# Performance work log

Measured on AMD Instinct MI355X. Metric: run time of the kernel, lower is better.

Reference implementation:

```python
import jax, jax.numpy as jnp
import numpy as np

TEMP = 1.0  # composition softmax temperature

def _bank_topk(x, U, V, logits, top_k):
    # softmax over primitive logits, select top-k, renormalize, fused low-rank projection
    w = jax.nn.softmax(logits / TEMP)                     # [P]
    tw, ti = jax.lax.top_k(w, top_k)                      # [k], [k]
    tw = tw / tw.sum()
    Us = U[ti]                                            # [k, d_in, r]
    Vs = V[ti]                                            # [k, r, d_out]
    h = jnp.einsum('bsd,kdr->bksr', x, Us)                # low-rank bottleneck
    return jnp.einsum('bksr,kro,k->bso', h, Vs, tw)       # weighted fuse

def reference(x, q_U, q_V, k_U, k_V, v_U, v_V, q_logits, k_logits, v_logits, out_w, top_k):
    B, S, _ = x.shape
    H, D = 16, 64
    q = _bank_topk(x, q_U, q_V, q_logits, top_k)
    k = _bank_topk(x, k_U, k_V, k_logits, top_k)
    v = _bank_topk(x, v_U, v_V, v_logits, top_k)
    q = q.reshape(B, S, H, D).transpose(0, 2, 1, 3)       # [B,H,S,D]
    k = k.reshape(B, S, H, D).transpose(0, 2, 1, 3)
    v = v.reshape(B, S, H, D).transpose(0, 2, 1, 3)
    scale = 1.0 / jnp.sqrt(jnp.asarray(D, dtype=x.dtype))
    scores = jnp.einsum('bhqd,bhkd->bhqk', q, k) * scale  # [B,H,S,S]
    causal = jnp.triu(jnp.ones((S, S), dtype=bool), 1)
    scores = jnp.where(causal[None, None], jnp.finfo(x.dtype).min, scores)
    probs = jax.nn.softmax(scores, axis=-1)
    out = jnp.einsum('bhqk,bhkd->bhqd', probs, v)
    out = out.transpose(0, 2, 1, 3).reshape(B, S, H * D)
    return out @ out_w.T                                   # nn.Linear(H*D, d_model, bias=False)

def setup_inputs() -> dict:
    key = jax.random.key(0)
    ks = jax.random.split(key, 11)
    P, d, r = 16, 1024, 64
    B, S = 4, 1024
    f = jnp.float32
    inp = {
        'x': jax.random.normal(ks[0], (B, S, d), f),
        'q_U': jax.random.normal(ks[1], (P, d, r), f) * (1.0 / np.sqrt(d)),
        'q_V': jax.random.normal(ks[2], (P, r, d), f) * (1.0 / np.sqrt(r)),
        'k_U': jax.random.normal(ks[3], (P, d, r), f) * (1.0 / np.sqrt(d)),
        'k_V': jax.random.normal(ks[4], (P, r, d), f) * (1.0 / np.sqrt(r)),
        'v_U': jax.random.normal(ks[5], (P, d, r), f) * (1.0 / np.sqrt(d)),
        'v_V': jax.random.normal(ks[6], (P, r, d), f) * (1.0 / np.sqrt(r)),
        'q_logits': jax.random.normal(ks[7], (P,), f) * 0.01,
        'k_logits': jax.random.normal(ks[8], (P,), f) * 0.01,
        'v_logits': jax.random.normal(ks[9], (P,), f) * 0.01,
        'out_w': jax.random.normal(ks[10], (d, d), f) * (1.0 / np.sqrt(d)),
        'top_k': 4,
    }
    return inp
```

## Files before the change

### kernel.cpp

```cpp
#include <hip/hip_runtime.h>
#include <math.h>

#define D_MODEL 1024
#define RANK    64
#define PMAX    16
#define S_LEN   1024
#define HD      64
#define MROWS   4096
#define NHEAD   16
#define BATCH   4
#define KCMAX   (PMAX * RANK)

typedef short short8v __attribute__((ext_vector_type(8)));
typedef short short4v __attribute__((ext_vector_type(4)));
typedef float floatx4 __attribute__((ext_vector_type(4)));

typedef __attribute__((address_space(1))) const unsigned int* gptr_t;
typedef __attribute__((address_space(3))) unsigned int* lptr_t;
typedef __attribute__((address_space(3))) short* lds3s;

static __device__ __forceinline__ void async16(const void* g, void* l) {
    __builtin_amdgcn_global_load_lds((gptr_t)g, (lptr_t)l, 16, 0, 0);
}

static __device__ __forceinline__ short f2bf(float f) {
    unsigned int u = __float_as_uint(f);
    u = (u + 0x7fffu + ((u >> 16) & 1u)) >> 16;
    return (short)u;
}

__global__ void topk_weights_kernel(const float* __restrict__ ql,
                                    const float* __restrict__ kl,
                                    const float* __restrict__ vl,
                                    const int* __restrict__ topk,
                                    int* __restrict__ idx_out,
                                    float* __restrict__ w_out) {
    int bank = threadIdx.x;
    if (bank >= 3) return;
    const float* lg = (bank == 0) ? ql : (bank == 1) ? kl : vl;
    int K = *topk; if (K < 1) K = 1; if (K > PMAX) K = PMAX;
    float l[PMAX];
    for (int i = 0; i < PMAX; ++i) l[i] = lg[i];
    bool used[PMAX];
    for (int i = 0; i < PMAX; ++i) used[i] = false;
    int   sel_i[PMAX];
    float sel_l[PMAX];
    for (int j = 0; j < K; ++j) {
        int best = -1; float bv = -INFINITY;
        for (int i = 0; i < PMAX; ++i)
            if (!used[i] && l[i] > bv) { bv = l[i]; best = i; }
        used[best] = true; sel_i[j] = best; sel_l[j] = bv;
    }
    float mx = sel_l[0];
    float e[PMAX];
    float sum = 0.f;
    for (int j = 0; j < K; ++j) { e[j] = __expf(sel_l[j] - mx); sum += e[j]; }
    float inv = 1.f / sum;
    for (int j = 0; j < PMAX; ++j) {
        idx_out[bank * PMAX + j] = (j < K) ? sel_i[j] : 0;
        w_out[bank * PMAX + j]   = (j < K) ? e[j] * inv : 0.f;
    }
}

__global__ __launch_bounds__(256) void convert_bf16_kernel(
    const float* __restrict__ src, short* __restrict__ dst, int n4) {
    int i = blockIdx.x * 256 + threadIdx.x;
    if (i < n4) {
        float4 f = ((const float4*)src)[i];
        short4 o;
        o.x = f2bf(f.x); o.y = f2bf(f.y); o.z = f2bf(f.z); o.w = f2bf(f.w);
        ((short4*)dst)[i] = o;
    }
}

__global__ __launch_bounds__(256) void prep_uv_kernel(
    const float* __restrict__ qU, const float* __restrict__ kU,
    const float* __restrict__ vU,
    const float* __restrict__ qV, const float* __restrict__ kV,
    const float* __restrict__ vV,
    const int* __restrict__ idx, const float* __restrict__ wsel,
    const int* __restrict__ topk,
    short* __restrict__ Uc, short* __restrict__ Vt) {
    int z    = blockIdx.z;
    int j    = blockIdx.y;
    int tile = blockIdx.x;
    int t    = threadIdx.x;
    int K = *topk; if (K < 1) K = 1; if (K > PMAX) K = PMAX;
    if (j >= K) return;
    __shared__ float T[64][65];
    int bank = (z < 3) ? z : z - 3;
    int p = idx[bank * PMAX + j];

    if (z < 3) {
        const float* U = (bank == 0) ? qU : (bank == 1) ? kU : vU;
        const float* src = U + (size_t)p * D_MODEL * RANK;
        short* dst = Uc + (size_t)bank * D_MODEL * KCMAX;
        int r4 = (t & 15) * 4;
        int dl = t >> 4;
#pragma unroll
        for (int i = 0; i < 4; ++i) {
            int d = tile * 64 + i * 16 + dl;
            float4 f = *(const float4*)&src[(size_t)d * RANK + r4];
            short4 o;
            o.x = f2bf(f.x); o.y = f2bf(f.y); o.z = f2bf(f.z); o.w = f2bf(f.w);
            *(short4*)&dst[(size_t)d * KCMAX + j * 64 + r4] = o;
        }
    } else {
        const float* V = (bank == 0) ? qV : (bank == 1) ? kV : vV;
        float wj = wsel[bank * PMAX + j];
        const float* src = V + (size_t)p * RANK * D_MODEL;
        int n0 = tile * 64;
        int nl = t & 63, rq = t >> 6;
#pragma unroll
        for (int i = 0; i < 16; ++i) {
            int rl = i * 4 + rq;
            T[nl][rl] = src[(size_t)rl * D_MODEL + n0 + nl] * wj;
        }
        __syncthreads();
        short* dst = Vt + (size_t)bank * D_MODEL * KCMAX;
        int rr = t >> 2;
#pragma unroll
        for (int i = 0; i < 4; ++i) {
            int c = (t & 3) * 16 + i * 4;
            short4 o;
            o.x = f2bf(T[rr][c + 0]); o.y = f2bf(T[rr][c + 1]);
            o.z = f2bf(T[rr][c + 2]); o.w = f2bf(T[rr][c + 3]);
            *(short4*)&dst[(size_t)(n0 + rr) * KCMAX + j * 64 + c] = o;
        }
    }
}

static __device__ __forceinline__ void mfma_gemm_tile(
    const short* __restrict__ A, const short* __restrict__ B, int kl,
    int lda, int ldb, int m0, int n0, short* As, short* Bs, floatx4 acc[4][4]) {
    const int t    = threadIdx.x;
    const int w    = t >> 6;
    const int lane = t & 63;
    const int wm   = w & 1, wn = w >> 1;
    const int colL = lane & 15, quad = lane >> 4;
    const int srow  = lane >> 2;
    const int skoff = (lane & 3) * 8;

#pragma unroll
    for (int i = 0; i < 4; ++i)
#pragma unroll
        for (int j = 0; j < 4; ++j) acc[i][j] = (floatx4){0.f, 0.f, 0.f, 0.f};

    for (int k0 = 0; k0 < kl; k0 += 32) {
        async16(A + (size_t)(m0 + w * 16 + srow) * lda + k0 + skoff,
                As + (w * 16 + srow) * 32 + skoff);
        async16(A + (size_t)(m0 + 64 + w * 16 + srow) * lda + k0 + skoff,
                As + (64 + w * 16 + srow) * 32 + skoff);
        async16(B + (size_t)(n0 + w * 16 + srow) * ldb + k0 + skoff,
                Bs + (w * 16 + srow) * 32 + skoff);
        async16(B + (size_t)(n0 + 64 + w * 16 + srow) * ldb + k0 + skoff,
                Bs + (64 + w * 16 + srow) * 32 + skoff);
        __syncthreads();
        short8v af[4], bf[4];
#pragma unroll
        for (int i = 0; i < 4; ++i)
            af[i] = *(const short8v*)&As[(wm * 64 + i * 16 + colL) * 32 + quad * 8];
#pragma unroll
        for (int j = 0; j < 4; ++j)
            bf[j] = *(const short8v*)&Bs[(wn * 64 + j * 16 + colL) * 32 + quad * 8];
#pragma unroll
        for (int i = 0; i < 4; ++i)
#pragma unroll
            for (int j = 0; j < 4; ++j)
                acc[i][j] = __builtin_amdgcn_mfma_f32_16x16x32_bf16(af[i], bf[j], acc[i][j], 0, 0, 0);
        __syncthreads();
    }
}

__global__ __launch_bounds__(256) void gemm_weff_kernel(
    const short* __restrict__ Vt, const short* __restrict__ Uc,
    const int* __restrict__ topk, short* __restrict__ Wt) {
    int K = *topk; if (K < 1) K = 1; if (K > PMAX) K = PMAX;
    int id = blockIdx.x + 8 * (blockIdx.y + 8 * blockIdx.z);
    int sw = (id & 7) * 24 + (id >> 3);
    int m0 = (sw & 7) * 128; int rest = sw >> 3;
    int n0 = (rest & 7) * 128; int bank = rest >> 3;
    __shared__ short As[128 * 32];
    __shared__ short Bs[128 * 32];
    floatx4 acc[4][4];
    mfma_gemm_tile(Vt + (size_t)bank * D_MODEL * KCMAX,
                   Uc + (size_t)bank * D_MODEL * KCMAX,
                   K * 64, KCMAX, KCMAX, m0, n0, As, Bs, acc);

    const int t = threadIdx.x, w = t >> 6, lane = t & 63;
    const int wm = w & 1, wn = w >> 1, colL = lane & 15, quad = lane >> 4;
    short* Wb = Wt + (size_t)bank * D_MODEL * D_MODEL;
#pragma unroll
    for (int i = 0; i < 4; ++i)
#pragma unroll
        for (int j = 0; j < 4; ++j)
#pragma unroll
            for (int r = 0; r < 4; ++r)
                Wb[(size_t)(m0 + wm * 64 + i * 16 + quad * 4 + r) * D_MODEL +
                   (n0 + wn * 64 + j * 16 + colL)] = f2bf(acc[i][j][r]);
}

__global__ __launch_bounds__(256) void gemm_qkv_kernel(
    const short* __restrict__ xb, const short* __restrict__ Wt,
    short* __restrict__ qkv) {
    int id = blockIdx.x + 32 * (blockIdx.y + 8 * blockIdx.z);
    int sw = (id & 7) * 96 + (id >> 3);
    int m0 = (sw & 31) * 128; int rest = sw >> 5;
    int n0 = (rest & 7) * 128; int bank = rest >> 3;
    __shared__ short As[128 * 32];
    __shared__ short Bs[128 * 32];
    floatx4 acc[4][4];
    mfma_gemm_tile(xb, Wt + (size_t)bank * D_MODEL * D_MODEL,
                   D_MODEL, D_MODEL, D_MODEL, m0, n0, As, Bs, acc);

    const int t = threadIdx.x, w = t >> 6, lane = t & 63;
    const int wm = w & 1, wn = w >> 1, colL = lane & 15, quad = lane >> 4;
    short* outp = qkv + (size_t)bank * MROWS * D_MODEL;
#pragma unroll
    for (int i = 0; i < 4; ++i)
#pragma unroll
        for (int j = 0; j < 4; ++j)
#pragma unroll
            for (int r = 0; r < 4; ++r) {
                int m = m0 + wm * 64 + i * 16 + quad * 4 + r;
                int n = n0 + wn * 64 + j * 16 + colL;
                int b = m >> 10, s = m & 1023;
                int head = n >> 6, d = n & 63;
                outp[(((size_t)(b * NHEAD + head) << 10) + s) * HD + d] = f2bf(acc[i][j][r]);
            }
}

__global__ __launch_bounds__(256) void gemm_proj_kernel(
    const short* __restrict__ attnb, const short* __restrict__ wb,
    float* __restrict__ outp) {
    int id = blockIdx.x + 32 * blockIdx.y;
    int sw = (id & 7) * 32 + (id >> 3);
    int m0 = (sw & 31) * 128;
    int n0 = (sw >> 5) * 128;
    __shared__ short As[128 * 32];
    __shared__ short Bs[128 * 32];
    floatx4 acc[4][4];
    mfma_gemm_tile(attnb, wb, D_MODEL, D_MODEL, D_MODEL, m0, n0, As, Bs, acc);

    const int t = threadIdx.x, w = t >> 6, lane = t & 63;
    const int wm = w & 1, wn = w >> 1, colL = lane & 15, quad = lane >> 4;
#pragma unroll
    for (int i = 0; i < 4; ++i)
#pragma unroll
        for (int j = 0; j < 4; ++j)
#pragma unroll
            for (int r = 0; r < 4; ++r)
                outp[(size_t)(m0 + wm * 64 + i * 16 + quad * 4 + r) * D_MODEL +
                     (n0 + wn * 64 + j * 16 + colL)] = acc[i][j][r];
}

__global__ __launch_bounds__(256) void attn_mfma_kernel(
    const short* __restrict__ qkv,
    short* __restrict__ attn_out) {
    const int t    = threadIdx.x;
    const int w    = t >> 6;
    const int lane = t & 63;
    const int col  = lane & 15;
    const int quad = lane >> 4;
    int id = blockIdx.x + 8 * blockIdx.y;
    int swz = (id & 7) * 64 + (id >> 3);
    const int pr = swz & 7;
    const int bh = swz >> 3;
    const size_t HS   = (size_t)S_LEN * HD;
    const size_t BSTR = (size_t)MROWS * D_MODEL;
    const short* Qg = qkv + (size_t)bh * HS;
    const short* Kg = qkv + BSTR + (size_t)bh * HS;
    const short* Vg = qkv + 2 * BSTR + (size_t)bh * HS;

    __shared__ short Ks[128 * 64];
    __shared__ short Vs[128 * 64];

    const float SC = 0.125f * 1.44269504f;

    int krow[4], kslot[4], vkey[4], voff[4];
#pragma unroll
    for (int it = 0; it < 4; ++it) {
        int c = t + it * 256;
        krow[it]  = c >> 3;
        kslot[it] = (c & 7) ^ ((c >> 3) & 7);
        int h = c & 1, kr = (c >> 1) & 3, k4 = (c >> 3) & 31, d16 = c >> 8;
        vkey[it] = k4 * 4 + kr;
        voff[it] = d16 * 16 + h * 8;
    }
    const int sw0 = (quad ^ (col & 7)) * 16;
    const int sw1 = ((4 + quad) ^ (col & 7)) * 16;
    lds3s vb = (lds3s)&Vs[quad * 64 + col * 4];

    for (int ph = 0; ph < 2; ++ph) {
        const int qt = ph ? (15 - pr) : pr;
        const int qb = qt * 4 + w;
        const int qrow = qt * 64 + w * 16 + col;
        short8v aq0 = *(const short8v*)(Qg + (size_t)qrow * HD + quad * 8);
        short8v aq1 = *(const short8v*)(Qg + (size_t)qrow * HD + 32 + quad * 8);
        floatx4 O0 = {0.f, 0.f, 0.f, 0.f}, O1 = O0, O2 = O0, O3 = O0;
        float mrow = -INFINITY, lrow = 0.f;
        const int nkv = (qt + 2) >> 1;

        for (int jt = 0; jt < nkv; ++jt) {
            __syncthreads();
#pragma unroll
            for (int it = 0; it < 4; ++it) {
                async16(Kg + (size_t)(jt * 128 + krow[it]) * HD + kslot[it] * 8,
                        Ks + (t + it * 256) * 8);
                async16(Vg + (size_t)(jt * 128 + vkey[it]) * HD + voff[it],
                        Vs + (t + it * 256) * 8);
            }
            __syncthreads();

            const int base = jt * 8;
            float s[8][4];
#pragma unroll
            for (int mb = 0; mb < 8; ++mb) {
                int rel = qb - (base + mb);
                if (rel >= 0) {
                    floatx4 c4 = {0.f, 0.f, 0.f, 0.f};
                    const char* kp = (const char*)Ks + mb * 2048 + col * 128;
                    short8v a0 = *(const short8v*)(kp + sw0);
                    short8v a1 = *(const short8v*)(kp + sw1);
                    c4 = __builtin_amdgcn_mfma_f32_16x16x32_bf16(a0, aq0, c4, 0, 0, 0);
                    c4 = __builtin_amdgcn_mfma_f32_16x16x32_bf16(a1, aq1, c4, 0, 0, 0);
#pragma unroll
                    for (int r = 0; r < 4; ++r) {
                        float v = c4[r] * SC;
                        if (rel == 0 && quad * 4 + r > col) v = -INFINITY;
                        s[mb][r] = v;
                    }
                } else {
#pragma unroll
                    for (int r = 0; r < 4; ++r) s[mb][r] = -INFINITY;
                }
            }
            float tm = -INFINITY;
#pragma unroll
            for (int mb = 0; mb < 8; ++mb)
#pragma unroll
                for (int r = 0; r < 4; ++r) tm = fmaxf(tm, s[mb][r]);
            tm = fmaxf(tm, __shfl_xor(tm, 16));
            tm = fmaxf(tm, __shfl_xor(tm, 32));
            if (__any(tm > mrow + 8.0f)) {
                float mnew  = fmaxf(mrow, tm);
                float alpha = exp2f(mrow - mnew);
                lrow *= alpha;
                mrow = mnew;
#pragma unroll
                for (int r = 0; r < 4; ++r) {
                    float ar = __shfl(alpha, quad * 4 + r);
                    O0[r] *= ar; O1[r] *= ar; O2[r] *= ar; O3[r] *= ar;
                }
            }
            float p[8][4];
            float ps = 0.f;
#pragma unroll
            for (int mb = 0; mb < 8; ++mb)
#pragma unroll
                for (int r = 0; r < 4; ++r) {
                    float e = exp2f(s[mb][r] - mrow);
                    p[mb][r] = e; ps += e;
                }
            ps += __shfl_xor(ps, 16);
            ps += __shfl_xor(ps, 32);
            lrow += ps;

            int lim = qb * 16 + 15 - (jt << 7);
            int ksm = lim >> 5; if (ksm > 3) ksm = 3;
#pragma unroll
            for (int ks = 0; ks < 4; ++ks) {
                if (ks <= ksm) {
                    lds3s vc = vb + ks * 512;
                    short4v t00, t01, t10, t11, t20, t21, t30, t31;
                    asm volatile("ds_read_b64_tr_b16 %0, %1" : "=v"(t00) : "v"(vc));
                    asm volatile("ds_read_b64_tr_b16 %0, %1" : "=v"(t01) : "v"(vc + 256));
                    asm volatile("ds_read_b64_tr_b16 %0, %1" : "=v"(t10) : "v"(vc + 2048));
                    asm volatile("ds_read_b64_tr_b16 %0, %1" : "=v"(t11) : "v"(vc + 2304));
                    asm volatile("ds_read_b64_tr_b16 %0, %1" : "=v"(t20) : "v"(vc + 4096));
                    asm volatile("ds_read_b64_tr_b16 %0, %1" : "=v"(t21) : "v"(vc + 4352));
                    asm volatile("ds_read_b64_tr_b16 %0, %1" : "=v"(t30) : "v"(vc + 6144));
                    asm volatile("ds_read_b64_tr_b16 %0, %1" : "=v"(t31) : "v"(vc + 6400));
                    short8v ap;
                    ap[0] = f2bf(p[2 * ks][0]);     ap[1] = f2bf(p[2 * ks][1]);
                    ap[2] = f2bf(p[2 * ks][2]);     ap[3] = f2bf(p[2 * ks][3]);
                    ap[4] = f2bf(p[2 * ks + 1][0]); ap[5] = f2bf(p[2 * ks + 1][1]);
                    ap[6] = f2bf(p[2 * ks + 1][2]); ap[7] = f2bf(p[2 * ks + 1][3]);
                    asm volatile("s_waitcnt lgkmcnt(0)" ::: "memory");
                    __builtin_amdgcn_sched_barrier(0);
                    short8v bv0 = __builtin_shufflevector(t00, t01, 0, 1, 2, 3, 4, 5, 6, 7);
                    short8v bv1 = __builtin_shufflevector(t10, t11, 0, 1, 2, 3, 4, 5, 6, 7);
                    short8v bv2 = __builtin_shufflevector(t20, t21, 0, 1, 2, 3, 4, 5, 6, 7);
                    short8v bv3 = __builtin_shufflevector(t30, t31, 0, 1, 2, 3, 4, 5, 6, 7);
                    O0 = __builtin_amdgcn_mfma_f32_16x16x32_bf16(ap, bv0, O0, 0, 0, 0);
                    O1 = __builtin_amdgcn_mfma_f32_16x16x32_bf16(ap, bv1, O1, 0, 0, 0);
                    O2 = __builtin_amdgcn_mfma_f32_16x16x32_bf16(ap, bv2, O2, 0, 0, 0);
                    O3 = __builtin_amdgcn_mfma_f32_16x16x32_bf16(ap, bv3, O3, 0, 0, 0);
                }
            }
        }
        const int b  = bh >> 4;
        const int hh = bh & 15;
        short* orow = attn_out +
            ((size_t)(b * S_LEN) + qt * 64 + w * 16) * D_MODEL + hh * 64;
        float linv = 1.f / lrow;
#pragma unroll
        for (int r = 0; r < 4; ++r) {
            float inv = __shfl(linv, quad * 4 + r);
            short* prw = orow + (size_t)(quad * 4 + r) * D_MODEL;
            prw[0  + col] = f2bf(O0[r] * inv);
            prw[16 + col] = f2bf(O1[r] * inv);
            prw[32 + col] = f2bf(O2[r] * inv);
            prw[48 + col] = f2bf(O3[r] * inv);
        }
    }
}

extern "C" void kernel_launch(void* const* d_in, const int* in_sizes, int n_in,
                              void* d_out, int out_size, void* d_ws, size_t ws_size,
                              hipStream_t stream) {
    const float* x    = (const float*)d_in[0];
    const float* qU   = (const float*)d_in[1];
    const float* qV   = (const float*)d_in[2];
    const float* kU   = (const float*)d_in[3];
    const float* kV   = (const float*)d_in[4];
    const float* vU   = (const float*)d_in[5];
    const float* vV   = (const float*)d_in[6];
    const float* qlg  = (const float*)d_in[7];
    const float* klg  = (const float*)d_in[8];
    const float* vlg  = (const float*)d_in[9];
    const float* outw = (const float*)d_in[10];
    const int*   topk = (const int*)d_in[11];
    float* outp = (float*)d_out;

    char* ws = (char*)d_ws;
    int*   idxp = (int*)ws;
    float* wp   = (float*)(ws + 256);
    short* xb   = (short*)(ws + 512);
    short* Uc   = xb + (size_t)MROWS * D_MODEL;
    short* Vt   = Uc + (size_t)3 * D_MODEL * KCMAX;
    short* wb   = Vt + (size_t)3 * D_MODEL * KCMAX;
    short* Wt   = wb + (size_t)D_MODEL * D_MODEL;
    short* qkvb = Wt + (size_t)3 * D_MODEL * D_MODEL;
    short* attnb = qkvb + (size_t)3 * MROWS * D_MODEL;

    topk_weights_kernel<<<1, 64, 0, stream>>>(qlg, klg, vlg, topk, idxp, wp);
    convert_bf16_kernel<<<(MROWS * D_MODEL / 4 + 255) / 256, 256, 0, stream>>>(
        x, xb, MROWS * D_MODEL / 4);
    convert_bf16_kernel<<<(D_MODEL * D_MODEL / 4 + 255) / 256, 256, 0, stream>>>(
        outw, wb, D_MODEL * D_MODEL / 4);
    prep_uv_kernel<<<dim3(16, 16, 6), 256, 0, stream>>>(
        qU, kU, vU, qV, kV, vV, idxp, wp, topk, Uc, Vt);
    gemm_weff_kernel<<<dim3(8, 8, 3), 256, 0, stream>>>(Vt, Uc, topk, Wt);
    gemm_qkv_kernel<<<dim3(32, 8, 3), 256, 0, stream>>>(xb, Wt, qkvb);
    attn_mfma_kernel<<<dim3(8, 64), 256, 0, stream>>>(qkvb, attnb);
    gemm_proj_kernel<<<dim3(32, 8), 256, 0, stream>>>(attnb, wb, outp);
}
```

Measured before the change: 211.9 us.

## Double-buffer attention K/V tiles and merge small prep kernels

The attention kernel now keeps two LDS buffers for K and V. The next tile is prefetched asynchronously while the current one is computed, with explicit vmcnt waits and barriers replacing the old load-then-sync pattern. The top-k softmax is recomputed redundantly inside each prep_uv block, which removes a separate tiny kernel launch, and the two bf16 conversion launches become one. The trade-off is double the LDS use for attention, which may lower occupancy, plus redundant top-k work in every prep block.

```diff
diff --git a/kernel.cpp b/kernel.cpp
--- a/kernel.cpp
+++ b/kernel.cpp
@@ -29,48 +29,25 @@
     return (short)u;
 }
 
-__global__ void topk_weights_kernel(const float* __restrict__ ql,
-                                    const float* __restrict__ kl,
-                                    const float* __restrict__ vl,
-                                    const int* __restrict__ topk,
-                                    int* __restrict__ idx_out,
-                                    float* __restrict__ w_out) {
-    int bank = threadIdx.x;
-    if (bank >= 3) return;
-    const float* lg = (bank == 0) ? ql : (bank == 1) ? kl : vl;
-    int K = *topk; if (K < 1) K = 1; if (K > PMAX) K = PMAX;
-    float l[PMAX];
-    for (int i = 0; i < PMAX; ++i) l[i] = lg[i];
-    bool used[PMAX];
-    for (int i = 0; i < PMAX; ++i) used[i] = false;
-    int   sel_i[PMAX];
-    float sel_l[PMAX];
-    for (int j = 0; j < K; ++j) {
-        int best = -1; float bv = -INFINITY;
-        for (int i = 0; i < PMAX; ++i)
-            if (!used[i] && l[i] > bv) { bv = l[i]; best = i; }
-        used[best] = true; sel_i[j] = best; sel_l[j] = bv;
-    }
-    float mx = sel_l[0];
-    float e[PMAX];
-    float sum = 0.f;
-    for (int j = 0; j < K; ++j) { e[j] = __expf(sel_l[j] - mx); sum += e[j]; }
-    float inv = 1.f / sum;
-    for (int j = 0; j < PMAX; ++j) {
-        idx_out[bank * PMAX + j] = (j < K) ? sel_i[j] : 0;
-        w_out[bank * PMAX + j]   = (j < K) ? e[j] * inv : 0.f;
-    }
-}
-
 __global__ __launch_bounds__(256) void convert_bf16_kernel(
-    const float* __restrict__ src, short* __restrict__ dst, int n4) {
+    const float* __restrict__ x, short* __restrict__ xb,
+    const float* __restrict__ w, short* __restrict__ wb) {
     int i = blockIdx.x * 256 + threadIdx.x;
-    if (i < n4) {
-        float4 f = ((const float4*)src)[i];
-        short4 o;
-        o.x = f2bf(f.x); o.y = f2bf(f.y); o.z = f2bf(f.z); o.w = f2bf(f.w);
-        ((short4*)dst)[i] = o;
-    }
+    const int NX = MROWS * D_MODEL / 4;
+    const int NW = D_MODEL * D_MODEL / 4;
+    const float* src;
+    short* dst;
+    if (i < NX) {
+        src = x; dst = xb;
+    } else {
+        i -= NX;
+        if (i >= NW) return;
+        src = w; dst = wb;
+    }
+    float4 f = ((const float4*)src)[i];
+    short4 o;
+    o.x = f2bf(f.x); o.y = f2bf(f.y); o.z = f2bf(f.z); o.w = f2bf(f.w);
+    ((short4*)dst)[i] = o;
 }
 
 __global__ __launch_bounds__(256) void prep_uv_kernel(
@@ -78,7 +55,8 @@
     const float* __restrict__ vU,
     const float* __restrict__ qV, const float* __restrict__ kV,
     const float* __restrict__ vV,
-    const int* __restrict__ idx, const float* __restrict__ wsel,
+    const float* __restrict__ ql, const float* __restrict__ kl,
+    const float* __restrict__ vl,
     const int* __restrict__ topk,
     short* __restrict__ Uc, short* __restrict__ Vt) {
     int z    = blockIdx.z;
@@ -89,7 +67,27 @@
     if (j >= K) return;
     __shared__ float T[64][65];
     int bank = (z < 3) ? z : z - 3;
-    int p = idx[bank * PMAX + j];
+
+    const float* lg = (bank == 0) ? ql : (bank == 1) ? kl : vl;
+    float l[PMAX];
+    bool used[PMAX];
+    for (int i = 0; i < PMAX; ++i) { l[i] = lg[i]; used[i] = false; }
+    int   si[PMAX];
+    float sl[PMAX];
+    for (int jj = 0; jj < K; ++jj) {
+        int best = -1; float bv = -INFINITY;
+        for (int i = 0; i < PMAX; ++i)
+            if (!used[i] && l[i] > bv) { bv = l[i]; best = i; }
+        used[best] = true; si[jj] = best; sl[jj] = bv;
+    }
+    float mx = sl[0], sum = 0.f, ej = 0.f;
+    for (int jj = 0; jj < K; ++jj) {
+        float e = __expf(sl[jj] - mx);
+        sum += e;
+        if (jj == j) ej = e;
+    }
+    int   p  = si[j];
+    float wj = ej / sum;
 
     if (z < 3) {
         const float* U = (bank == 0) ? qU : (bank == 1) ? kU : vU;
@@ -107,7 +105,6 @@
         }
     } else {
         const float* V = (bank == 0) ? qV : (bank == 1) ? kV : vV;
-        float wj = wsel[bank * PMAX + j];
         const float* src = V + (size_t)p * RANK * D_MODEL;
         int n0 = tile * 64;
         int nl = t & 63, rq = t >> 6;
@@ -272,8 +269,8 @@
     const short* Kg = qkv + BSTR + (size_t)bh * HS;
     const short* Vg = qkv + 2 * BSTR + (size_t)bh * HS;
 
-    __shared__ short Ks[128 * 64];
-    __shared__ short Vs[128 * 64];
+    __shared__ short Ks[2][128 * 64];
+    __shared__ short Vs[2][128 * 64];
 
     const float SC = 0.125f * 1.44269504f;
 
@@ -289,7 +286,17 @@
     }
     const int sw0 = (quad ^ (col & 7)) * 16;
     const int sw1 = ((4 + quad) ^ (col & 7)) * 16;
-    lds3s vb = (lds3s)&Vs[quad * 64 + col * 4];
+    lds3s vb = (lds3s)&Vs[0][quad * 64 + col * 4];
+
+    auto STAGE = [&](int buf, int jt) {
+#pragma unroll
+        for (int it = 0; it < 4; ++it) {
+            async16(Kg + (size_t)(jt * 128 + krow[it]) * HD + kslot[it] * 8,
+                    &Ks[buf][(t + it * 256) * 8]);
+            async16(Vg + (size_t)(jt * 128 + vkey[it]) * HD + voff[it],
+                    &Vs[buf][(t + it * 256) * 8]);
+        }
+    };
 
     for (int ph = 0; ph < 2; ++ph) {
         const int qt = ph ? (15 - pr) : pr;
@@ -297,20 +304,26 @@
         const int qrow = qt * 64 + w * 16 + col;
         short8v aq0 = *(const short8v*)(Qg + (size_t)qrow * HD + quad * 8);
         short8v aq1 = *(const short8v*)(Qg + (size_t)qrow * HD + 32 + quad * 8);
+        asm volatile("s_waitcnt vmcnt(0)" : "+v"(aq0), "+v"(aq1) :: "memory");
         floatx4 O0 = {0.f, 0.f, 0.f, 0.f}, O1 = O0, O2 = O0, O3 = O0;
         float mrow = -INFINITY, lrow = 0.f;
         const int nkv = (qt + 2) >> 1;
 
+        STAGE(0, 0);
+        int cur = 0;
         for (int jt = 0; jt < nkv; ++jt) {
-            __syncthreads();
-#pragma unroll
-            for (int it = 0; it < 4; ++it) {
-                async16(Kg + (size_t)(jt * 128 + krow[it]) * HD + kslot[it] * 8,
-                        Ks + (t + it * 256) * 8);
-                async16(Vg + (size_t)(jt * 128 + vkey[it]) * HD + voff[it],
-                        Vs + (t + it * 256) * 8);
+            __builtin_amdgcn_sched_barrier(0);
+            if (jt + 1 < nkv) {
+                STAGE(cur ^ 1, jt + 1);
+                asm volatile("s_waitcnt vmcnt(8)" ::: "memory");
+            } else {
+                asm volatile("s_waitcnt vmcnt(0)" ::: "memory");
             }
-            __syncthreads();
+            __builtin_amdgcn_s_barrier();
+            __builtin_amdgcn_sched_barrier(0);
+
+            const short* Kb = &Ks[cur][0];
+            lds3s vbc = vb + cur * (128 * 64);
 
             const int base = jt * 8;
             float s[8][4];
@@ -319,7 +332,7 @@
                 int rel = qb - (base + mb);
                 if (rel >= 0) {
                     floatx4 c4 = {0.f, 0.f, 0.f, 0.f};
-                    const char* kp = (const char*)Ks + mb * 2048 + col * 128;
+                    const char* kp = (const char*)Kb + mb * 2048 + col * 128;
                     short8v a0 = *(const short8v*)(kp + sw0);
                     short8v a1 = *(const short8v*)(kp + sw1);
                     c4 = __builtin_amdgcn_mfma_f32_16x16x32_bf16(a0, aq0, c4, 0, 0, 0);
@@ -371,7 +384,7 @@
 #pragma unroll
             for (int ks = 0; ks < 4; ++ks) {
                 if (ks <= ksm) {
-                    lds3s vc = vb + ks * 512;
+                    lds3s vc = vbc + ks * 512;
                     short4v t00, t01, t10, t11, t20, t21, t30, t31;
                     asm volatile("ds_read_b64_tr_b16 %0, %1" : "=v"(t00) : "v"(vc));
                     asm volatile("ds_read_b64_tr_b16 %0, %1" : "=v"(t01) : "v"(vc + 256));
@@ -398,6 +411,9 @@
                     O3 = __builtin_amdgcn_mfma_f32_16x16x32_bf16(ap, bv3, O3, 0, 0, 0);
                 }
             }
+            __builtin_amdgcn_sched_barrier(0);
+            __builtin_amdgcn_s_barrier();
+            cur ^= 1;
         }
         const int b  = bh >> 4;
         const int hh = bh & 15;
@@ -434,8 +450,6 @@
     float* outp = (float*)d_out;
 
     char* ws = (char*)d_ws;
-    int*   idxp = (int*)ws;
-    float* wp   = (float*)(ws + 256);
     short* xb   = (short*)(ws + 512);
     short* Uc   = xb + (size_t)MROWS * D_MODEL;
     short* Vt   = Uc + (size_t)3 * D_MODEL * KCMAX;
@@ -444,13 +458,10 @@
     short* qkvb = Wt + (size_t)3 * D_MODEL * D_MODEL;
     short* attnb = qkvb + (size_t)3 * MROWS * D_MODEL;
 
-    topk_weights_kernel<<<1, 64, 0, stream>>>(qlg, klg, vlg, topk, idxp, wp);
-    convert_bf16_kernel<<<(MROWS * D_MODEL / 4 + 255) / 256, 256, 0, stream>>>(
-        x, xb, MROWS * D_MODEL / 4);
-    convert_bf16_kernel<<<(D_MODEL * D_MODEL / 4 + 255) / 256, 256, 0, stream>>>(
-        outw, wb, D_MODEL * D_MODEL / 4);
+    const int NCV = (MROWS * D_MODEL + D_MODEL * D_MODEL) / 4 / 256;
+    convert_bf16_kernel<<<NCV, 256, 0, stream>>>(x, xb, outw, wb);
     prep_uv_kernel<<<dim3(16, 16, 6), 256, 0, stream>>>(
-        qU, kU, vU, qV, kV, vV, idxp, wp, topk, Uc, Vt);
+        qU, kU, vU, qV, kV, vV, qlg, klg, vlg, topk, Uc, Vt);
     gemm_weff_kernel<<<dim3(8, 8, 3), 256, 0, stream>>>(Vt, Uc, topk, Wt);
     gemm_qkv_kernel<<<dim3(32, 8, 3), 256, 0, stream>>>(xb, Wt, qkvb);
     attn_mfma_kernel<<<dim3(8, 64), 256, 0, stream>>>(qkvb, attnb);
```

Measured after the change: 227.8 us. 7.5% more time.
